# Performance work log

Hardware: AMD Instinct MI355X
Metric: run time of the kernel (lower is better)

## Reference

```python
import jax, jax.numpy as jnp
import numpy as np

N, C, H, W = 8, 128, 128, 128   # batch, emb channels, spatial
O, M, K, L = 81, 1, 3, 3        # classes, num_modes, neg_num_modes, neg MPC layers
SIGMA, BETA, NEG_SCOPE = 0.5, 0.3, 2.0
EPS = 1e-12


def _l2norm(v, axis):
    # matches F.normalize: v / max(||v||, eps)
    n = jnp.sqrt(jnp.sum(v * v, axis=axis, keepdims=True))
    return v / jnp.maximum(n, EPS)


def setup_inputs() -> dict:
    key = jax.random.key(0)
    k0, k1, k2 = jax.random.split(key, 3)
    return {
        "x": jax.random.normal(k0, (N, C, H, W), jnp.float32),
        "rep_fc_w": jax.random.normal(k1, (O * M * C,), jnp.float32) * 0.01,
        "rep_fc_b": jnp.zeros((O * M * C,), jnp.float32),
        "neg_w": jax.random.normal(k2, (K, L, C, C), jnp.float32) * 0.01,
        "neg_b": jnp.zeros((K, L, C), jnp.float32),
    }


def reference(x, rep_fc_w, rep_fc_b, neg_w, neg_b):
    # emb_module = identity; L2-normalize embeddings over channel dim
    e = _l2norm(x, axis=1)                      # (N,C,H,W)
    ehw = e.transpose(0, 2, 3, 1)               # (N,H,W,C)

    # reps = rep_fc(1.0) -> weight + bias (Linear(1, O*M*C) applied to scalar 1)
    reps = (rep_fc_w + rep_fc_b).reshape(O, M, C)
    reps = _l2norm(reps, axis=2)                # (O,1,C) unit rows

    # negative reps: K independent 3-layer MLPs (ReLU between layers)
    r = reps[:, 0, :]                           # (O,C)
    neg_list = []
    for k in range(K):
        h = r
        for l in range(L):
            h = h @ neg_w[k, l].T + neg_b[k, l]
            if l < L - 1:
                h = jax.nn.relu(h)
        neg_list.append(h)
    reps_neg = jnp.stack(neg_list, axis=1)      # (O,K,C)
    reps_neg = _l2norm(reps_neg, axis=2)

    # Both sides unit-norm -> ||e - r||^2 = 2 - 2<e,r>; compute via GEMM
    dot = jnp.einsum('nhwc,omc->nomhw', ehw, reps)        # (N,O,M,H,W)
    distances = jnp.sqrt(jax.nn.relu(2.0 - 2.0 * dot))
    dot_n = jnp.einsum('nhwc,okc->nokhw', ehw, reps_neg)  # (N,O,K,H,W)
    distances_neg = jnp.sqrt(jax.nn.relu(2.0 - 2.0 * dot_n))

    inv = 1.0 / (2.0 * SIGMA ** 2)
    probs_neg = jnp.exp(-distances_neg ** 2 * inv)
    cls_score_neg = probs_neg.max(axis=2)                 # (N,O,H,W)

    probs_ori = jnp.exp(-distances ** 2 * inv).max(axis=2)  # (N,O,H,W)

    min_neg = distances_neg.min(axis=2, keepdims=True)    # (N,O,1,H,W)
    probs = jnp.exp(-(distances + BETA * jax.nn.relu(NEG_SCOPE - min_neg)) ** 2 * inv)

    # cls_norm = True: normalize summed probs over classes
    probs_sumj = probs.sum(axis=2)                        # (N,O,H,W)
    cls_score = probs_sumj / probs_sumj.sum(axis=1, keepdims=True)

    return (cls_score, cls_score_neg, distances, distances_neg, probs_ori)
```

## Files before the change

### kernel.cpp

```cpp
#include <hip/hip_runtime.h>

#define HW 16384

typedef short bf16x8 __attribute__((ext_vector_type(8)));
typedef float f32x4 __attribute__((ext_vector_type(4)));

static constexpr size_t OFF0 = 0;
static constexpr size_t OFF1 = 10616832;
static constexpr size_t OFF2 = 21233664;
static constexpr size_t OFF3 = 31850496;
static constexpr size_t OFF4 = 63700992;

#define STG_STRIDE 264

static __device__ __forceinline__ unsigned short f2bf(float f) {
  unsigned int u = __float_as_uint(f);
  u += 0x7fffu + ((u >> 16) & 1u);
  return (unsigned short)(u >> 16);
}

static __device__ __forceinline__ void frag_write(unsigned short* wsA, int R, int j,
                                                  unsigned short v) {
  const int mt = R >> 4;
  const int ks = j >> 5;
  const int hi = (j >> 3) & 3;
  const int jj = j & 7;
  const int lane = hi * 16 + (R & 15);
  wsA[((size_t)((mt * 4 + ks) * 64 + lane)) * 8 + jj] = v;
}

__global__ __launch_bounds__(128) void prep_all(const float* __restrict__ rw,
                                                const float* __restrict__ rb,
                                                const float* __restrict__ nw,
                                                const float* __restrict__ nb,
                                                unsigned short* __restrict__ wsA) {
  const int b = blockIdx.x;
  const int k = b / 81, o = b % 81;
  const int j = threadIdx.x;
  __shared__ __align__(16) float hrow[128];
  __shared__ float red[2];

  float v = rw[o * 128 + j] + rb[o * 128 + j];
  float sq = v * v;
#pragma unroll
  for (int m = 1; m < 64; m <<= 1) sq += __shfl_xor(sq, m, 64);
  if ((j & 63) == 0) red[j >> 6] = sq;
  __syncthreads();
  const float r = v / fmaxf(sqrtf(red[0] + red[1]), 1e-12f);
  __syncthreads();
  hrow[j] = r;
  __syncthreads();

  float acc = 0.f;
#pragma unroll
  for (int l = 0; l < 3; ++l) {
    const float4* Wr = (const float4*)(nw + (((size_t)(k * 3 + l)) * 128 + j) * 128);
    const float4* H  = (const float4*)hrow;
    float4 a = {0.f, 0.f, 0.f, 0.f};
#pragma unroll
    for (int q = 0; q < 32; ++q) {
      float4 wv = Wr[q]; float4 hv = H[q];
      a.x = fmaf(wv.x, hv.x, a.x); a.y = fmaf(wv.y, hv.y, a.y);
      a.z = fmaf(wv.z, hv.z, a.z); a.w = fmaf(wv.w, hv.w, a.w);
    }
    acc = (a.x + a.y) + (a.z + a.w) + nb[(k * 3 + l) * 128 + j];
    if (l < 2) acc = fmaxf(acc, 0.f);
    __syncthreads();
    if (l < 2) hrow[j] = acc;
    __syncthreads();
  }

  float sq2 = acc * acc;
#pragma unroll
  for (int m = 1; m < 64; m <<= 1) sq2 += __shfl_xor(sq2, m, 64);
  if ((j & 63) == 0) red[j >> 6] = sq2;
  __syncthreads();
  const float accn = acc / fmaxf(sqrtf(red[0] + red[1]), 1e-12f);

  frag_write(wsA, o * 4 + k + 1, j, f2bf(accn));
  if (k == 0) frag_write(wsA, o * 4, j, f2bf(r));
  if (b == 0) {
#pragma unroll
    for (int R = 324; R < 336; ++R) frag_write(wsA, R, j, (unsigned short)0);
  }
}

__global__ __launch_bounds__(512, 4) void main_kernel(const float* __restrict__ x,
                                                      const bf16x8* __restrict__ wsA,
                                                      float* __restrict__ out) {
  __shared__ __align__(16) char lds[74752];
  float* ss   = (float*)(lds + 65536);
  float* invn = (float*)(lds + 73728);
  float* stg  = (float*)lds;

  const int b = blockIdx.x;
  const int n = b >> 6;
  const int p0 = (b & 63) << 8;
  const int t = threadIdx.x;
  const int lane = t & 63;
  const int w = t >> 6;
  const float* xb = x + ((size_t)n * 128) * HW + p0;

  {
    const int pq = (t & 63) * 4;
    const int swz = (t & 7) << 4;
    float a0 = 0.f, a1 = 0.f, a2 = 0.f, a3 = 0.f;
#pragma unroll
    for (int i = 0; i < 4; ++i) {
      const int c0 = i * 32 + w * 4;
      float4 v0 = *(const float4*)(xb + (size_t)(c0 + 0) * HW + pq);
      float4 v1 = *(const float4*)(xb + (size_t)(c0 + 1) * HW + pq);
      float4 v2 = *(const float4*)(xb + (size_t)(c0 + 2) * HW + pq);
      float4 v3 = *(const float4*)(xb + (size_t)(c0 + 3) * HW + pq);
      a0 = fmaf(v0.x, v0.x, fmaf(v1.x, v1.x, fmaf(v2.x, v2.x, fmaf(v3.x, v3.x, a0))));
      a1 = fmaf(v0.y, v0.y, fmaf(v1.y, v1.y, fmaf(v2.y, v2.y, fmaf(v3.y, v3.y, a1))));
      a2 = fmaf(v0.z, v0.z, fmaf(v1.z, v1.z, fmaf(v2.z, v2.z, fmaf(v3.z, v3.z, a2))));
      a3 = fmaf(v0.w, v0.w, fmaf(v1.w, v1.w, fmaf(v2.w, v2.w, fmaf(v3.w, v3.w, a3))));
      uint2 wd;
      wd.x = (unsigned)f2bf(v0.x) | ((unsigned)f2bf(v1.x) << 16);
      wd.y = (unsigned)f2bf(v2.x) | ((unsigned)f2bf(v3.x) << 16);
      *(uint2*)(lds + (((pq + 0) * 256 + c0 * 2) ^ swz)) = wd;
      wd.x = (unsigned)f2bf(v0.y) | ((unsigned)f2bf(v1.y) << 16);
      wd.y = (unsigned)f2bf(v2.y) | ((unsigned)f2bf(v3.y) << 16);
      *(uint2*)(lds + (((pq + 1) * 256 + c0 * 2) ^ swz)) = wd;
      wd.x = (unsigned)f2bf(v0.z) | ((unsigned)f2bf(v1.z) << 16);
      wd.y = (unsigned)f2bf(v2.z) | ((unsigned)f2bf(v3.z) << 16);
      *(uint2*)(lds + (((pq + 2) * 256 + c0 * 2) ^ swz)) = wd;
      wd.x = (unsigned)f2bf(v0.w) | ((unsigned)f2bf(v1.w) << 16);
      wd.y = (unsigned)f2bf(v2.w) | ((unsigned)f2bf(v3.w) << 16);
      *(uint2*)(lds + (((pq + 3) * 256 + c0 * 2) ^ swz)) = wd;
    }
    float4 st = {a0, a1, a2, a3};
    *(float4*)&ss[w * 256 + pq] = st;
  }
  __syncthreads();
  if (t < 256) {
    float s = 0.f;
#pragma unroll
    for (int g = 0; g < 8; ++g) s += ss[g * 256 + t];
    invn[t] = __builtin_amdgcn_rsqf(fmaxf(s, 1e-24f));
  }
  __syncthreads();

  const int og = lane >> 4;
  const int px16 = lane & 15;

  bf16x8 bfrag[2][4];
  float ivp[2];
#pragma unroll
  for (int u = 0; u < 2; ++u) {
    const int p = w * 32 + u * 16 + px16;
    const int swzr = ((p >> 2) & 7) << 4;
#pragma unroll
    for (int ks = 0; ks < 4; ++ks) {
      const int addr = (p * 256 + ks * 64 + (lane >> 4) * 16) ^ swzr;
      bfrag[u][ks] = *(const bf16x8*)(lds + addr);
    }
    ivp[u] = invn[p];
  }
  __syncthreads();

  unsigned probs_pk[21];

#pragma unroll
  for (int mt = 0; mt < 21; ++mt) {
    bf16x8 afr[4];
#pragma unroll
    for (int ks = 0; ks < 4; ++ks) afr[ks] = wsA[(mt * 4 + ks) * 64 + lane];
    f32x4 c0 = {0.f, 0.f, 0.f, 0.f}, c1 = {0.f, 0.f, 0.f, 0.f};
#pragma unroll
    for (int ks = 0; ks < 4; ++ks) {
      c0 = __builtin_amdgcn_mfma_f32_16x16x32_bf16(afr[ks], bfrag[0][ks], c0, 0, 0, 0);
      c1 = __builtin_amdgcn_mfma_f32_16x16x32_bf16(afr[ks], bfrag[1][ks], c1, 0, 0, 0);
    }
    const int o = mt * 4 + og;
    const bool valid = (o < 81);
    float pru[2];
#pragma unroll
    for (int u = 0; u < 2; ++u) {
      const f32x4 c = u ? c1 : c0;
      const float iv = ivp[u];
      float q0 = fmaxf(2.f - 2.f * (c[0] * iv), 0.f);
      float q1 = fmaxf(2.f - 2.f * (c[1] * iv), 0.f);
      float q2 = fmaxf(2.f - 2.f * (c[2] * iv), 0.f);
      float q3 = fmaxf(2.f - 2.f * (c[3] * iv), 0.f);
      float d0 = __builtin_amdgcn_sqrtf(q0);
      float d1 = __builtin_amdgcn_sqrtf(q1);
      float d2 = __builtin_amdgcn_sqrtf(q2);
      float d3 = __builtin_amdgcn_sqrtf(q3);
      float qmin = fminf(q1, fminf(q2, q3));
      float dmin = fminf(d1, fminf(d2, d3));
      float pneg = __expf(-2.f * qmin);
      float pori = __expf(-2.f * q0);
      float tt = d0 + 0.3f * fmaxf(2.f - dmin, 0.f);
      float pr = __expf(-2.f * tt * tt);
      pru[u] = valid ? pr : 0.f;
      float* su = stg + og * 6 * STG_STRIDE + w * 32 + u * 16 + px16;
      su[0] = d0;
      su[1 * STG_STRIDE] = d1;
      su[2 * STG_STRIDE] = d2;
      su[3 * STG_STRIDE] = d3;
      su[4 * STG_STRIDE] = pneg;
      su[5 * STG_STRIDE] = pori;
    }
    probs_pk[mt] = ((unsigned)f2bf(pru[1]) << 16) | (unsigned)f2bf(pru[0]);
    __syncthreads();
#pragma unroll
    for (int r = 0; r < 3; ++r) {
      const int m = w * 3 + r;
      const int ogm = m / 6, jv = m % 6;
      const int oo = mt * 4 + ogm;
      f32x4 v = *(const f32x4*)(stg + m * STG_STRIDE + lane * 4);
      if (oo < 81) {
        const size_t idx81 = (size_t)(n * 81 + oo);
        size_t off;
        if (jv == 0) off = OFF2 + idx81 * HW;
        else if (jv <= 3) off = OFF3 + (idx81 * 3 + (jv - 1)) * HW;
        else if (jv == 4) off = OFF1 + idx81 * HW;
        else off = OFF4 + idx81 * HW;
        __builtin_nontemporal_store(v, (f32x4*)(out + off + p0 + lane * 4));
      }
    }
    __syncthreads();
  }

  float s0 = 0.f, s1 = 0.f;
#pragma unroll
  for (int mt = 0; mt < 21; ++mt) {
    s0 += __uint_as_float(probs_pk[mt] << 16);
    s1 += __uint_as_float(probs_pk[mt] & 0xffff0000u);
  }
  s0 += __shfl_xor(s0, 16, 64); s0 += __shfl_xor(s0, 32, 64);
  s1 += __shfl_xor(s1, 16, 64); s1 += __shfl_xor(s1, 32, 64);
  const float is0 = __builtin_amdgcn_rcpf(s0);
  const float is1 = __builtin_amdgcn_rcpf(s1);

#pragma unroll
  for (int g = 0; g < 4; ++g) {
    const int nj = (g < 3) ? 6 : 3;
#pragma unroll
    for (int j = 0; j < 6; ++j) {
      if (j < nj) {
        const int mt = g * 6 + j;
        const float v0 = __uint_as_float(probs_pk[mt] << 16) * is0;
        const float v1 = __uint_as_float(probs_pk[mt] & 0xffff0000u) * is1;
        float* su = stg + (j * 4 + og) * STG_STRIDE + w * 32 + px16;
        su[0] = v0;
        su[16] = v1;
      }
    }
    __syncthreads();
    const int nrows = nj * 4;
#pragma unroll
    for (int r = 0; r < 3; ++r) {
      const int m = w * 3 + r;
      if (m < nrows) {
        const int j = m >> 2, ogm = m & 3;
        const int oo = (g * 6 + j) * 4 + ogm;
        f32x4 v = *(const f32x4*)(stg + m * STG_STRIDE + lane * 4);
        if (oo < 81) {
          __builtin_nontemporal_store(
              v, (f32x4*)(out + OFF0 + (size_t)(n * 81 + oo) * HW + p0 + lane * 4));
        }
      }
    }
    __syncthreads();
  }
}

extern "C" void kernel_launch(void* const* d_in, const int* in_sizes, int n_in,
                              void* d_out, int out_size, void* d_ws, size_t ws_size,
                              hipStream_t stream) {
  const float* x  = (const float*)d_in[0];
  const float* rw = (const float*)d_in[1];
  const float* rb = (const float*)d_in[2];
  const float* nw = (const float*)d_in[3];
  const float* nb = (const float*)d_in[4];
  float* out = (float*)d_out;
  unsigned short* wsA_us = (unsigned short*)d_ws;
  const bf16x8* wsA = (const bf16x8*)d_ws;

  hipLaunchKernelGGL(prep_all, dim3(243), dim3(128), 0, stream, rw, rb, nw, nb, wsA_us);
  hipLaunchKernelGGL(main_kernel, dim3(512), dim3(512), 0, stream, x, wsA, out);
}
```

Before: 104.1 us.

## Double pixel tile per block to 512 and halve grid

Each block now handles 512 pixels instead of 256, so each wave computes four 16-pixel MFMA column tiles per class tile and reuses every A-fragment load across twice as many pixels. The grid shrinks from 512 to 256 blocks, LDS grows to about 138KB, and the occupancy hint of 4 is removed. Staging, normalization and output stores are reworked for the wider tile. Fewer blocks than CUs and the larger LDS footprint may reduce latency hiding on a store-bound kernel.

```diff
diff --git a/kernel.cpp b/kernel.cpp
--- a/kernel.cpp
+++ b/kernel.cpp
@@ -11,12 +11,19 @@
 static constexpr size_t OFF3 = 31850496;
 static constexpr size_t OFF4 = 63700992;
 
-#define STG_STRIDE 264
+#define STRIDE 520
 
 static __device__ __forceinline__ unsigned short f2bf(float f) {
   unsigned int u = __float_as_uint(f);
   u += 0x7fffu + ((u >> 16) & 1u);
   return (unsigned short)(u >> 16);
+}
+
+static __device__ __forceinline__ float bflo(unsigned pk) {
+  return __uint_as_float(pk << 16);
+}
+static __device__ __forceinline__ float bfhi(unsigned pk) {
+  return __uint_as_float(pk & 0xffff0000u);
 }
 
 static __device__ __forceinline__ void frag_write(unsigned short* wsA, int R, int j,
@@ -85,29 +92,30 @@
   }
 }
 
-__global__ __launch_bounds__(512, 4) void main_kernel(const float* __restrict__ x,
-                                                      const bf16x8* __restrict__ wsA,
-                                                      float* __restrict__ out) {
-  __shared__ __align__(16) char lds[74752];
-  float* ss   = (float*)(lds + 65536);
-  float* invn = (float*)(lds + 73728);
+__global__ __launch_bounds__(512) void main_kernel(const float* __restrict__ x,
+                                                   const bf16x8* __restrict__ wsA,
+                                                   float* __restrict__ out) {
+  __shared__ __align__(16) char lds[141312];
+  float* ss   = (float*)(lds + 131072);
+  float* invn = (float*)(lds + 139264);
   float* stg  = (float*)lds;
 
   const int b = blockIdx.x;
-  const int n = b >> 6;
-  const int p0 = (b & 63) << 8;
+  const int n = b >> 5;
+  const int p0 = (b & 31) << 9;
   const int t = threadIdx.x;
   const int lane = t & 63;
   const int w = t >> 6;
   const float* xb = x + ((size_t)n * 128) * HW + p0;
 
   {
-    const int pq = (t & 63) * 4;
+    const int pq = (t & 127) * 4;
+    const int cg = t >> 7;
     const int swz = (t & 7) << 4;
     float a0 = 0.f, a1 = 0.f, a2 = 0.f, a3 = 0.f;
 #pragma unroll
-    for (int i = 0; i < 4; ++i) {
-      const int c0 = i * 32 + w * 4;
+    for (int i = 0; i < 8; ++i) {
+      const int c0 = i * 16 + cg * 4;
       float4 v0 = *(const float4*)(xb + (size_t)(c0 + 0) * HW + pq);
       float4 v1 = *(const float4*)(xb + (size_t)(c0 + 1) * HW + pq);
       float4 v2 = *(const float4*)(xb + (size_t)(c0 + 2) * HW + pq);
@@ -131,13 +139,11 @@
       *(uint2*)(lds + (((pq + 3) * 256 + c0 * 2) ^ swz)) = wd;
     }
     float4 st = {a0, a1, a2, a3};
-    *(float4*)&ss[w * 256 + pq] = st;
-  }
-  __syncthreads();
-  if (t < 256) {
-    float s = 0.f;
-#pragma unroll
-    for (int g = 0; g < 8; ++g) s += ss[g * 256 + t];
+    *(float4*)&ss[cg * 512 + pq] = st;
+  }
+  __syncthreads();
+  {
+    float s = ss[t] + ss[512 + t] + ss[1024 + t] + ss[1536 + t];
     invn[t] = __builtin_amdgcn_rsqf(fmaxf(s, 1e-24f));
   }
   __syncthreads();
@@ -145,11 +151,11 @@
   const int og = lane >> 4;
   const int px16 = lane & 15;
 
-  bf16x8 bfrag[2][4];
-  float ivp[2];
-#pragma unroll
-  for (int u = 0; u < 2; ++u) {
-    const int p = w * 32 + u * 16 + px16;
+  bf16x8 bfrag[4][4];
+  float ivp[4];
+#pragma unroll
+  for (int u = 0; u < 4; ++u) {
+    const int p = w * 64 + u * 16 + px16;
     const int swzr = ((p >> 2) & 7) << 4;
 #pragma unroll
     for (int ks = 0; ks < 4; ++ks) {
@@ -160,25 +166,28 @@
   }
   __syncthreads();
 
-  unsigned probs_pk[21];
+  unsigned p01[21], p23[21];
 
 #pragma unroll
   for (int mt = 0; mt < 21; ++mt) {
     bf16x8 afr[4];
 #pragma unroll
     for (int ks = 0; ks < 4; ++ks) afr[ks] = wsA[(mt * 4 + ks) * 64 + lane];
-    f32x4 c0 = {0.f, 0.f, 0.f, 0.f}, c1 = {0.f, 0.f, 0.f, 0.f};
+    f32x4 cc[4];
+#pragma unroll
+    for (int u = 0; u < 4; ++u) cc[u] = (f32x4){0.f, 0.f, 0.f, 0.f};
 #pragma unroll
     for (int ks = 0; ks < 4; ++ks) {
-      c0 = __builtin_amdgcn_mfma_f32_16x16x32_bf16(afr[ks], bfrag[0][ks], c0, 0, 0, 0);
-      c1 = __builtin_amdgcn_mfma_f32_16x16x32_bf16(afr[ks], bfrag[1][ks], c1, 0, 0, 0);
+#pragma unroll
+      for (int u = 0; u < 4; ++u)
+        cc[u] = __builtin_amdgcn_mfma_f32_16x16x32_bf16(afr[ks], bfrag[u][ks], cc[u], 0, 0, 0);
     }
     const int o = mt * 4 + og;
     const bool valid = (o < 81);
-    float pru[2];
-#pragma unroll
-    for (int u = 0; u < 2; ++u) {
-      const f32x4 c = u ? c1 : c0;
+    float pr_[4];
+#pragma unroll
+    for (int u = 0; u < 4; ++u) {
+      const f32x4 c = cc[u];
       const float iv = ivp[u];
       float q0 = fmaxf(2.f - 2.f * (c[0] * iv), 0.f);
       float q1 = fmaxf(2.f - 2.f * (c[1] * iv), 0.f);
@@ -194,23 +203,25 @@
       float pori = __expf(-2.f * q0);
       float tt = d0 + 0.3f * fmaxf(2.f - dmin, 0.f);
       float pr = __expf(-2.f * tt * tt);
-      pru[u] = valid ? pr : 0.f;
-      float* su = stg + og * 6 * STG_STRIDE + w * 32 + u * 16 + px16;
-      su[0] = d0;
-      su[1 * STG_STRIDE] = d1;
-      su[2 * STG_STRIDE] = d2;
-      su[3 * STG_STRIDE] = d3;
-      su[4 * STG_STRIDE] = pneg;
-      su[5 * STG_STRIDE] = pori;
-    }
-    probs_pk[mt] = ((unsigned)f2bf(pru[1]) << 16) | (unsigned)f2bf(pru[0]);
+      pr_[u] = valid ? pr : 0.f;
+      float* su = stg + og * 6 * STRIDE + w * 64 + u * 16 + px16;
+      su[0 * STRIDE] = d0;
+      su[1 * STRIDE] = d1;
+      su[2 * STRIDE] = d2;
+      su[3 * STRIDE] = d3;
+      su[4 * STRIDE] = pneg;
+      su[5 * STRIDE] = pori;
+    }
+    p01[mt] = ((unsigned)f2bf(pr_[1]) << 16) | (unsigned)f2bf(pr_[0]);
+    p23[mt] = ((unsigned)f2bf(pr_[3]) << 16) | (unsigned)f2bf(pr_[2]);
     __syncthreads();
 #pragma unroll
     for (int r = 0; r < 3; ++r) {
       const int m = w * 3 + r;
       const int ogm = m / 6, jv = m % 6;
       const int oo = mt * 4 + ogm;
-      f32x4 v = *(const f32x4*)(stg + m * STG_STRIDE + lane * 4);
+      f32x4 h0 = *(const f32x4*)(stg + m * STRIDE + lane * 4);
+      f32x4 h1 = *(const f32x4*)(stg + m * STRIDE + 256 + lane * 4);
       if (oo < 81) {
         const size_t idx81 = (size_t)(n * 81 + oo);
         size_t off;
@@ -218,49 +229,56 @@
         else if (jv <= 3) off = OFF3 + (idx81 * 3 + (jv - 1)) * HW;
         else if (jv == 4) off = OFF1 + idx81 * HW;
         else off = OFF4 + idx81 * HW;
-        __builtin_nontemporal_store(v, (f32x4*)(out + off + p0 + lane * 4));
+        __builtin_nontemporal_store(h0, (f32x4*)(out + off + p0 + lane * 4));
+        __builtin_nontemporal_store(h1, (f32x4*)(out + off + p0 + 256 + lane * 4));
       }
     }
     __syncthreads();
   }
 
-  float s0 = 0.f, s1 = 0.f;
+  float s0 = 0.f, s1 = 0.f, s2 = 0.f, s3 = 0.f;
 #pragma unroll
   for (int mt = 0; mt < 21; ++mt) {
-    s0 += __uint_as_float(probs_pk[mt] << 16);
-    s1 += __uint_as_float(probs_pk[mt] & 0xffff0000u);
+    s0 += bflo(p01[mt]); s1 += bfhi(p01[mt]);
+    s2 += bflo(p23[mt]); s3 += bfhi(p23[mt]);
   }
   s0 += __shfl_xor(s0, 16, 64); s0 += __shfl_xor(s0, 32, 64);
   s1 += __shfl_xor(s1, 16, 64); s1 += __shfl_xor(s1, 32, 64);
+  s2 += __shfl_xor(s2, 16, 64); s2 += __shfl_xor(s2, 32, 64);
+  s3 += __shfl_xor(s3, 16, 64); s3 += __shfl_xor(s3, 32, 64);
   const float is0 = __builtin_amdgcn_rcpf(s0);
   const float is1 = __builtin_amdgcn_rcpf(s1);
-
-#pragma unroll
-  for (int g = 0; g < 4; ++g) {
-    const int nj = (g < 3) ? 6 : 3;
-#pragma unroll
-    for (int j = 0; j < 6; ++j) {
-      if (j < nj) {
-        const int mt = g * 6 + j;
-        const float v0 = __uint_as_float(probs_pk[mt] << 16) * is0;
-        const float v1 = __uint_as_float(probs_pk[mt] & 0xffff0000u) * is1;
-        float* su = stg + (j * 4 + og) * STG_STRIDE + w * 32 + px16;
-        su[0] = v0;
-        su[16] = v1;
+  const float is2 = __builtin_amdgcn_rcpf(s2);
+  const float is3 = __builtin_amdgcn_rcpf(s3);
+
+#pragma unroll
+  for (int g = 0; g < 6; ++g) {
+    const int nmt = (g < 5) ? 4 : 1;
+#pragma unroll
+    for (int mtl = 0; mtl < 4; ++mtl) {
+      if (mtl < nmt) {
+        const int mt = g * 4 + mtl;
+        float* su = stg + (mtl * 4 + og) * STRIDE + w * 64 + px16;
+        su[0]  = bflo(p01[mt]) * is0;
+        su[16] = bfhi(p01[mt]) * is1;
+        su[32] = bflo(p23[mt]) * is2;
+        su[48] = bfhi(p23[mt]) * is3;
       }
     }
     __syncthreads();
-    const int nrows = nj * 4;
-#pragma unroll
-    for (int r = 0; r < 3; ++r) {
-      const int m = w * 3 + r;
+    const int nrows = nmt * 4;
+#pragma unroll
+    for (int r = 0; r < 2; ++r) {
+      const int m = w * 2 + r;
       if (m < nrows) {
-        const int j = m >> 2, ogm = m & 3;
-        const int oo = (g * 6 + j) * 4 + ogm;
-        f32x4 v = *(const f32x4*)(stg + m * STG_STRIDE + lane * 4);
+        const int mtl = m >> 2, ogm = m & 3;
+        const int oo = (g * 4 + mtl) * 4 + ogm;
+        f32x4 h0 = *(const f32x4*)(stg + m * STRIDE + lane * 4);
+        f32x4 h1 = *(const f32x4*)(stg + m * STRIDE + 256 + lane * 4);
         if (oo < 81) {
-          __builtin_nontemporal_store(
-              v, (f32x4*)(out + OFF0 + (size_t)(n * 81 + oo) * HW + p0 + lane * 4));
+          const size_t off = OFF0 + (size_t)(n * 81 + oo) * HW;
+          __builtin_nontemporal_store(h0, (f32x4*)(out + off + p0 + lane * 4));
+          __builtin_nontemporal_store(h1, (f32x4*)(out + off + p0 + 256 + lane * 4));
         }
       }
     }
@@ -281,5 +299,5 @@
   const bf16x8* wsA = (const bf16x8*)d_ws;
 
   hipLaunchKernelGGL(prep_all, dim3(243), dim3(128), 0, stream, rw, rb, nw, nb, wsA_us);
-  hipLaunchKernelGGL(main_kernel, dim3(512), dim3(512), 0, stream, x, wsA, out);
-}
+  hipLaunchKernelGGL(main_kernel, dim3(256), dim3(512), 0, stream, x, wsA, out);
+}
```

New measurement: 108.9 us. +4.6%, slower.
